# Kernel optimization log

Measured on AMD Instinct MI355X. Metric: run time of the kernel, lower is better.

Reference implementation:

```python
import jax, jax.numpy as jnp
import numpy as np

T, H, I, E, TOP_K = 1024, 1024, 512, 16, 4
SHARED_I = 512  # moe_intermediate_size * n_shared_experts


def setup_inputs() -> dict:
    key = jax.random.key(0)
    ks = jax.random.split(key, 6)
    s = 0.02
    return {
        "hidden_states": jax.random.normal(ks[0], (T, H), dtype=jnp.float32),
        "gate_w": jax.random.normal(ks[1], (E, H), dtype=jnp.float32) * s,          # router weight
        "w_gate_up": jax.random.normal(ks[2], (E, H, 2 * I), dtype=jnp.float32) * s,  # per-expert merged gate/up
        "w_down": jax.random.normal(ks[3], (E, I, H), dtype=jnp.float32) * s,
        "shared_gate_up": jax.random.normal(ks[4], (H, 2 * SHARED_I), dtype=jnp.float32) * s,
        "shared_down": jax.random.normal(ks[5], (SHARED_I, H), dtype=jnp.float32) * s,
    }


def _swiglu(gu):
    g, u = jnp.split(gu, 2, axis=-1)  # gate first, then up (SiluAndMul)
    return jax.nn.silu(g) * u


def reference(hidden_states, gate_w, w_gate_up, w_down, shared_gate_up, shared_down):
    x = hidden_states  # [T, H]
    # ---- router: sigmoid scoring, plain top-k (num_expert_group=topk_group=1), renormalize ----
    logits = x @ gate_w.T                      # [T, E]
    scores = jax.nn.sigmoid(logits)            # [T, E]
    topk_vals, topk_idx = jax.lax.top_k(scores, TOP_K)
    topk_w = topk_vals / jnp.sum(topk_vals, axis=-1, keepdims=True)
    # dense routing matrix [T, E] (zeros for unselected experts)
    route = jnp.zeros_like(scores).at[jnp.arange(T)[:, None], topk_idx].set(topk_w)
    # ---- routed experts: grouped SwiGLU GEMMs, combined by routing weights ----
    gu = jnp.einsum('th,ehf->etf', x, w_gate_up)   # [E, T, 2I]
    h = _swiglu(gu)                                 # [E, T, I]
    eo = jnp.einsum('eti,eih->eth', h, w_down)      # [E, T, H]
    routed = jnp.einsum('te,eth->th', route, eo)    # [T, H]
    # ---- shared expert (routed_scaling_factor = 1.0) ----
    shared = _swiglu(x @ shared_gate_up) @ shared_down  # [T, H]
    return routed + shared
```

## Files before the change

### kernel.cpp

```cpp
#include <hip/hip_runtime.h>
#include <hip/hip_bf16.h>
#include <cstdint>

#define T_TOK 1024
#define H_DIM 1024
#define I_DIM 512
#define E_NUM 16
#define TOPK  4

typedef __bf16 bf16;
typedef __bf16 bf16x4 __attribute__((ext_vector_type(4)));
typedef __bf16 bf16x8 __attribute__((ext_vector_type(8)));
typedef float  f32x4  __attribute__((ext_vector_type(4)));

#define GLOAD16(g, l)                                                                   \
  __builtin_amdgcn_global_load_lds((const __attribute__((address_space(1))) void*)(g),  \
                                   (__attribute__((address_space(3))) void*)(l), 16, 0, 0)

__device__ __forceinline__ unsigned lds_addr(const bf16* p) {
  return (unsigned)(uintptr_t)(const __attribute__((address_space(3))) bf16*)p;
}

template <int OFF>
__device__ __forceinline__ bf16x4 tr_read(unsigned addr) {
  bf16x4 r;
  if constexpr (OFF == 0)
    asm volatile("ds_read_b64_tr_b16 %0, %1" : "=v"(r) : "v"(addr));
  else if constexpr (OFF == 512)
    asm volatile("ds_read_b64_tr_b16 %0, %1 offset:512" : "=v"(r) : "v"(addr));
  else
    asm volatile("ds_read_b64_tr_b16 %0, %1 offset:1024" : "=v"(r) : "v"(addr));
  return r;
}

__device__ __forceinline__ bf16x8 cat8(bf16x4 a, bf16x4 b) {
  return __builtin_shufflevector(a, b, 0, 1, 2, 3, 4, 5, 6, 7);
}

__device__ __forceinline__ void conv_task(const float* __restrict__ src,
                                          bf16* __restrict__ dst, int lt, int tid) {
  const size_t b4 = (size_t)lt * 2048 + 2 * tid;
  const float4* s4 = (const float4*)src;
  float4 fa[4], fb[4];
#pragma unroll
  for (int p = 0; p < 4; ++p) {
    fa[p] = s4[b4 + (size_t)p * 512];
    fb[p] = s4[b4 + (size_t)p * 512 + 1];
  }
  bf16x8* d8 = (bf16x8*)dst;
#pragma unroll
  for (int p = 0; p < 4; ++p) {
    bf16x8 o;
    o[0]=(bf16)fa[p].x; o[1]=(bf16)fa[p].y; o[2]=(bf16)fa[p].z; o[3]=(bf16)fa[p].w;
    o[4]=(bf16)fb[p].x; o[5]=(bf16)fb[p].y; o[6]=(bf16)fb[p].z; o[7]=(bf16)fb[p].w;
    d8[(size_t)lt * 1024 + tid + (size_t)p * 256] = o;
  }
}

__global__ void prep_kernel(const float* __restrict__ x, bf16* __restrict__ xb,
                            const float* __restrict__ wgu, bf16* __restrict__ wguB,
                            const float* __restrict__ sgu, bf16* __restrict__ sguB,
                            const float* __restrict__ gw,
                            int* __restrict__ topk_e, float* __restrict__ topk_w,
                            int* __restrict__ counts, int* __restrict__ tok,
                            float* __restrict__ wt, int* __restrict__ slot) {
  const int b = blockIdx.x, tid = threadIdx.x;
  if (b < 1152) {
#pragma unroll
    for (int it = 0; it < 2; ++it) {
      const int task = b + it * 1152;
      if (task < 2048)      conv_task(wgu, wguB, task, tid);
      else if (task < 2176) conv_task(sgu, sguB, task - 2048, tid);
      else                  conv_task(x, xb, task - 2176, tid);
    }
  } else if (b < 1408) {
    const int wave = tid >> 6, lane = tid & 63;
    const int t = (b - 1152) * 4 + wave;
    const float4* xr = (const float4*)(x + (size_t)t * H_DIM);
    float4 xv[4];
#pragma unroll
    for (int j = 0; j < 4; ++j) xv[j] = xr[lane + 64 * j];
    float p[E_NUM];
#pragma unroll
    for (int e = 0; e < E_NUM; ++e) {
      const float4* gr = (const float4*)(gw + (size_t)e * H_DIM);
      float s = 0.f;
#pragma unroll
      for (int j = 0; j < 4; ++j) {
        float4 g = gr[lane + 64 * j];
        s += xv[j].x * g.x + xv[j].y * g.y + xv[j].z * g.z + xv[j].w * g.w;
      }
      p[e] = s;
    }
#pragma unroll
    for (int off = 32; off > 0; off >>= 1) {
#pragma unroll
      for (int e = 0; e < E_NUM; ++e) p[e] += __shfl_xor(p[e], off);
    }
    float rem[E_NUM];
#pragma unroll
    for (int e = 0; e < E_NUM; ++e) rem[e] = 1.f / (1.f + __expf(-p[e]));
    float vals[TOPK]; int idx[TOPK];
#pragma unroll
    for (int k = 0; k < TOPK; ++k) {
      float m = rem[0]; int mi = 0;
#pragma unroll
      for (int e = 1; e < E_NUM; ++e) {
        if (rem[e] > m) { m = rem[e]; mi = e; }
      }
      vals[k] = m; idx[k] = mi;
#pragma unroll
      for (int e = 0; e < E_NUM; ++e) rem[e] = (e == mi) ? -1e30f : rem[e];
    }
    if (lane == 0) {
      float inv = 1.f / (vals[0] + vals[1] + vals[2] + vals[3]);
      int4 ids; ids.x = idx[0]; ids.y = idx[1]; ids.z = idx[2]; ids.w = idx[3];
      float4 w4; w4.x = vals[0]*inv; w4.y = vals[1]*inv; w4.z = vals[2]*inv; w4.w = vals[3]*inv;
      ((int4*)topk_e)[t] = ids;
      ((float4*)topk_w)[t] = w4;
    }
  } else {
    const int i = (b - 1408) * 256 + tid;
    if (i == 0) counts[E_NUM] = T_TOK;
    tok [E_NUM * T_TOK + i] = i;
    wt  [E_NUM * T_TOK + i] = 1.0f;
    slot[E_NUM * T_TOK + i] = T_TOK * TOPK + i;
  }
}

__global__ void router_build_kernel(const int* __restrict__ topk_e, const float* __restrict__ topk_w,
                                    int* __restrict__ counts, int* __restrict__ tok,
                                    float* __restrict__ wt, int* __restrict__ slot) {
  const int e = blockIdx.x;
  const int tid = threadIdx.x, wave = tid >> 6, lane = tid & 63;
  __shared__ int wsum[4];
  int base = 0;
  for (int r = 0; r < 4; ++r) {
    int t = r * 256 + tid;
    int4 ids = ((const int4*)topk_e)[t];
    int match = -1;
    if (ids.x == e) match = 0;
    if (ids.y == e) match = 1;
    if (ids.z == e) match = 2;
    if (ids.w == e) match = 3;
    unsigned long long bm = __ballot(match >= 0);
    int prefix = __popcll(bm & ((1ull << lane) - 1ull));
    if (lane == 0) wsum[wave] = __popcll(bm);
    __syncthreads();
    int wbase = 0;
#pragma unroll
    for (int wv = 0; wv < 4; ++wv) wbase += (wv < wave) ? wsum[wv] : 0;
    int total = wsum[0] + wsum[1] + wsum[2] + wsum[3];
    if (match >= 0) {
      int pos = base + wbase + prefix;
      tok [e * T_TOK + pos] = t;
      wt  [e * T_TOK + pos] = topk_w[t * 4 + match];
      slot[e * T_TOK + pos] = t * 4 + match;
    }
    base += total;
    __syncthreads();
  }
  if (tid == 0) counts[e] = base;
}

__global__ __launch_bounds__(256, 4)
void gemm1_kernel(const bf16* __restrict__ xb, const bf16* __restrict__ wguB,
                  const bf16* __restrict__ sguB, const int* __restrict__ counts,
                  const int* __restrict__ tok, const float* __restrict__ wt,
                  const int* __restrict__ slot, bf16* __restrict__ hbuf,
                  const float* __restrict__ wdF, bf16* __restrict__ wdBo,
                  const float* __restrict__ sdF, bf16* __restrict__ sdBo) {
  const int tid = threadIdx.x;
  const int e = blockIdx.z;
  if (e >= 17) {
    const int cid = (e - 17) * 128 + blockIdx.y * 8 + blockIdx.x;
    if (cid < 1024)      conv_task(wdF, wdBo, cid, tid);
    else if (cid < 1088) conv_task(sdF, sdBo, cid - 1024, tid);
    return;
  }
  const int cnt = counts[e];
  const int rt  = blockIdx.y;
  if (rt * 64 >= cnt) return;
  const int nb = blockIdx.x * 64;
  const bf16* WB = (e < E_NUM) ? (wguB + (size_t)e * H_DIM * (2 * I_DIM)) : sguB;

  __shared__ __align__(16) bf16 sA[3][64 * 32];
  __shared__ __align__(16) bf16 sG[3][2048];
  __shared__ __align__(16) bf16 sU[3][2048];

  const int wave = tid >> 6, lane = tid & 63;
  const int wr = wave >> 1, wc = wave & 1;
  const int fr = lane & 15, kg = lane >> 4;
  const int lr = lane >> 2, lk = (lane & 3) * 8;

  int ar = rt * 64 + wave * 16 + lr;
  int arc = ar < cnt ? ar : cnt - 1;
  const bf16* aS = xb + (size_t)tok[e * T_TOK + arc] * H_DIM + lk;
  const int aOff = wave * 512;

  const int k_off = 8 * wave + 4 * (lane >> 5) + ((lane & 7) >> 1);
  const int n_off = 16 * ((lane >> 3) & 3) + 8 * (lane & 1);
  const bf16* gS = WB + (size_t)k_off * (2 * I_DIM) + nb + n_off;
  const bf16* uS = WB + (size_t)k_off * (2 * I_DIM) + I_DIM + nb + n_off;
  const int wOff = wave * 512;

  f32x4 accg[2][2], accu[2][2];
#pragma unroll
  for (int i = 0; i < 2; ++i)
#pragma unroll
    for (int j = 0; j < 2; ++j) { accg[i][j] = f32x4{0,0,0,0}; accu[i][j] = f32x4{0,0,0,0}; }

#define STG1(t, bidx) do { size_t ko = (size_t)(t) * 32;    \
    GLOAD16(aS + ko, sA[bidx] + aOff);                      \
    GLOAD16(gS + ko * (2 * I_DIM), sG[bidx] + wOff);        \
    GLOAD16(uS + ko * (2 * I_DIM), sU[bidx] + wOff); } while (0)

  STG1(0, 0); STG1(1, 1);
  const int NT = H_DIM / 32;
  int bufc = 0;
  for (int t = 0; t < NT; ++t) {
    int bn = bufc + 2; bn = bn >= 3 ? bn - 3 : bn;
    if (t + 2 < NT) {
      STG1(t + 2, bn);
      asm volatile("s_waitcnt vmcnt(6)" ::: "memory");
    } else if (t + 1 < NT) {
      asm volatile("s_waitcnt vmcnt(3)" ::: "memory");
    } else {
      asm volatile("s_waitcnt vmcnt(0)" ::: "memory");
    }
    __builtin_amdgcn_s_barrier();
    __builtin_amdgcn_sched_barrier(0);
    const bf16* A = sA[bufc];
    bf16x8 a0 = *(const bf16x8*)(A + (wr * 32      + fr) * 32 + kg * 8);
    bf16x8 a1 = *(const bf16x8*)(A + (wr * 32 + 16 + fr) * 32 + kg * 8);
    unsigned gb = lds_addr(sG[bufc]) + (unsigned)((lane >> 4) << 10) + (unsigned)((lane & 15) << 3);
    unsigned ub = lds_addr(sU[bufc]) + (unsigned)((lane >> 4) << 10) + (unsigned)((lane & 15) << 3);
    unsigned nb0 = (unsigned)(wc * 256), nb1 = nb0 + 128;
    bf16x8 g0 = cat8(tr_read<0>(gb + nb0), tr_read<512>(gb + nb0));
    bf16x8 g1 = cat8(tr_read<0>(gb + nb1), tr_read<512>(gb + nb1));
    bf16x8 u0 = cat8(tr_read<0>(ub + nb0), tr_read<512>(ub + nb0));
    bf16x8 u1 = cat8(tr_read<0>(ub + nb1), tr_read<512>(ub + nb1));
    asm volatile("s_waitcnt lgkmcnt(0)" ::: "memory");
    __builtin_amdgcn_sched_barrier(0);
    __builtin_amdgcn_s_setprio(1);
    accg[0][0] = __builtin_amdgcn_mfma_f32_16x16x32_bf16(a0, g0, accg[0][0], 0, 0, 0);
    accg[0][1] = __builtin_amdgcn_mfma_f32_16x16x32_bf16(a0, g1, accg[0][1], 0, 0, 0);
    accg[1][0] = __builtin_amdgcn_mfma_f32_16x16x32_bf16(a1, g0, accg[1][0], 0, 0, 0);
    accg[1][1] = __builtin_amdgcn_mfma_f32_16x16x32_bf16(a1, g1, accg[1][1], 0, 0, 0);
    accu[0][0] = __builtin_amdgcn_mfma_f32_16x16x32_bf16(a0, u0, accu[0][0], 0, 0, 0);
    accu[0][1] = __builtin_amdgcn_mfma_f32_16x16x32_bf16(a0, u1, accu[0][1], 0, 0, 0);
    accu[1][0] = __builtin_amdgcn_mfma_f32_16x16x32_bf16(a1, u0, accu[1][0], 0, 0, 0);
    accu[1][1] = __builtin_amdgcn_mfma_f32_16x16x32_bf16(a1, u1, accu[1][1], 0, 0, 0);
    __builtin_amdgcn_s_setprio(0);
    __builtin_amdgcn_sched_barrier(0);
    __builtin_amdgcn_s_barrier();
    bufc = bufc == 2 ? 0 : bufc + 1;
  }
#undef STG1

#pragma unroll
  for (int mi = 0; mi < 2; ++mi) {
#pragma unroll
    for (int j = 0; j < 4; ++j) {
      int grow = rt * 64 + wr * 32 + mi * 16 + kg * 4 + j;
      if (grow < cnt) {
        bf16* hr = hbuf + (size_t)slot[e * T_TOK + grow] * I_DIM;
        float w = wt[e * T_TOK + grow];
#pragma unroll
        for (int ni = 0; ni < 2; ++ni) {
          float g = accg[mi][ni][j], u = accu[mi][ni][j];
          float h = w * (g / (1.f + __expf(-g))) * u;
          hr[nb + wc * 32 + ni * 16 + fr] = (bf16)h;
        }
      }
    }
  }
}

__global__ __launch_bounds__(256, 4)
void gemm2_kernel(const bf16* __restrict__ hbuf, const bf16* __restrict__ wdB,
                  const bf16* __restrict__ sdB, const int* __restrict__ counts,
                  const int* __restrict__ slot, bf16* __restrict__ obuf) {
  const int e   = blockIdx.z;
  const int cnt = counts[e];
  const int rt  = blockIdx.y;
  if (rt * 64 >= cnt) return;
  const int nb = blockIdx.x * 128;
  const bf16* WB = (e < E_NUM) ? (wdB + (size_t)e * I_DIM * H_DIM) : sdB;

  __shared__ __align__(16) bf16 sA[3][64 * 32];
  __shared__ __align__(16) bf16 sB[3][4096];

  const int tid = threadIdx.x, wave = tid >> 6, lane = tid & 63;
  const int wr = wave >> 1, wc = wave & 1;
  const int fr = lane & 15, kg = lane >> 4;
  const int lr = lane >> 2, lk = (lane & 3) * 8;

  int ar = rt * 64 + wave * 16 + lr;
  int arc = ar < cnt ? ar : cnt - 1;
  const bf16* aS = hbuf + (size_t)slot[e * T_TOK + arc] * I_DIM + lk;
  const int aOff = wave * 512;

  const int j2 = (lane & 7) >> 1, h2 = lane & 1, nblk2 = lane >> 3;
  const int n2 = nb + nblk2 * 16 + 8 * h2;
  const bf16* bS0 = WB + (size_t)((wave * 2 + 0) * 4 + j2) * H_DIM + n2;
  const bf16* bS1 = WB + (size_t)((wave * 2 + 1) * 4 + j2) * H_DIM + n2;
  const int bOff0 = wave * 1024;
  const int bOff1 = bOff0 + 512;

  f32x4 acc[2][4];
#pragma unroll
  for (int i = 0; i < 2; ++i)
#pragma unroll
    for (int j = 0; j < 4; ++j) acc[i][j] = f32x4{0,0,0,0};

#define STG2(t, bidx) do { size_t ko = (size_t)(t) * 32;    \
    GLOAD16(aS + ko, sA[bidx] + aOff);                      \
    GLOAD16(bS0 + ko * H_DIM, sB[bidx] + bOff0);            \
    GLOAD16(bS1 + ko * H_DIM, sB[bidx] + bOff1); } while (0)

  STG2(0, 0); STG2(1, 1);
  const int NT = I_DIM / 32;
  int bufc = 0;
  for (int t = 0; t < NT; ++t) {
    int bn = bufc + 2; bn = bn >= 3 ? bn - 3 : bn;
    if (t + 2 < NT) {
      STG2(t + 2, bn);
      asm volatile("s_waitcnt vmcnt(6)" ::: "memory");
    } else if (t + 1 < NT) {
      asm volatile("s_waitcnt vmcnt(3)" ::: "memory");
    } else {
      asm volatile("s_waitcnt vmcnt(0)" ::: "memory");
    }
    __builtin_amdgcn_s_barrier();
    __builtin_amdgcn_sched_barrier(0);
    const bf16* A = sA[bufc];
    bf16x8 a0 = *(const bf16x8*)(A + (wr * 32      + fr) * 32 + kg * 8);
    bf16x8 a1 = *(const bf16x8*)(A + (wr * 32 + 16 + fr) * 32 + kg * 8);
    unsigned bb = lds_addr(sB[bufc]) + (unsigned)((lane >> 4) << 11) + (unsigned)((lane & 15) << 3)
                + (unsigned)(wc * 512);
    bf16x8 b[4];
#pragma unroll
    for (int ni = 0; ni < 4; ++ni)
      b[ni] = cat8(tr_read<0>(bb + ni * 128), tr_read<1024>(bb + ni * 128));
    asm volatile("s_waitcnt lgkmcnt(0)" ::: "memory");
    __builtin_amdgcn_sched_barrier(0);
    __builtin_amdgcn_s_setprio(1);
#pragma unroll
    for (int ni = 0; ni < 4; ++ni) {
      acc[0][ni] = __builtin_amdgcn_mfma_f32_16x16x32_bf16(a0, b[ni], acc[0][ni], 0, 0, 0);
      acc[1][ni] = __builtin_amdgcn_mfma_f32_16x16x32_bf16(a1, b[ni], acc[1][ni], 0, 0, 0);
    }
    __builtin_amdgcn_s_setprio(0);
    __builtin_amdgcn_sched_barrier(0);
    __builtin_amdgcn_s_barrier();
    bufc = bufc == 2 ? 0 : bufc + 1;
  }
#undef STG2

#pragma unroll
  for (int mi = 0; mi < 2; ++mi) {
#pragma unroll
    for (int j = 0; j < 4; ++j) {
      int grow = rt * 64 + wr * 32 + mi * 16 + kg * 4 + j;
      if (grow < cnt) {
        bf16* orow = obuf + (size_t)slot[e * T_TOK + grow] * H_DIM + nb + wc * 64 + fr;
#pragma unroll
        for (int ni = 0; ni < 4; ++ni)
          orow[ni * 16] = (bf16)acc[mi][ni][j];
      }
    }
  }
}

__global__ void reduce_kernel(const bf16* __restrict__ obuf, float* __restrict__ out) {
  const int t = blockIdx.x;
  const int c = threadIdx.x;
  const bf16x4* o4 = (const bf16x4*)obuf;
  float4 s; s.x = s.y = s.z = s.w = 0.f;
  int rows[5] = {t * 4, t * 4 + 1, t * 4 + 2, t * 4 + 3, T_TOK * TOPK + t};
#pragma unroll
  for (int r = 0; r < 5; ++r) {
    bf16x4 v = o4[(size_t)rows[r] * 256 + c];
    s.x += (float)v[0]; s.y += (float)v[1]; s.z += (float)v[2]; s.w += (float)v[3];
  }
  ((float4*)out)[(size_t)t * 256 + c] = s;
}

extern "C" void kernel_launch(void* const* d_in, const int* in_sizes, int n_in,
                              void* d_out, int out_size, void* d_ws, size_t ws_size,
                              hipStream_t stream) {
  const float* x   = (const float*)d_in[0];
  const float* gw  = (const float*)d_in[1];
  const float* wgu = (const float*)d_in[2];
  const float* wd  = (const float*)d_in[3];
  const float* sgu = (const float*)d_in[4];
  const float* sd  = (const float*)d_in[5];
  float* out = (float*)d_out;

  char* ws = (char*)d_ws;
  int*   counts = (int*)  (ws);
  int*   tok    = (int*)  (ws + 1024);
  float* wtA    = (float*)(ws + 70656);
  int*   slotA  = (int*)  (ws + 140288);
  int*   topk_e = (int*)  (ws + 209920);
  float* topk_w = (float*)(ws + 226304);
  bf16*  xb     = (bf16*) (ws + 245760);
  bf16*  hbuf   = (bf16*) (ws + 2342912);
  bf16*  wguB   = (bf16*) (ws + 7585792);
  bf16*  wdB    = (bf16*) (ws + 41140224);
  bf16*  sguB   = (bf16*) (ws + 57917440);
  bf16*  sdB    = (bf16*) (ws + 60014592);
  bf16*  obuf   = (bf16*) (ws + 7585792);

  prep_kernel<<<1412, 256, 0, stream>>>(x, xb, wgu, wguB, sgu, sguB,
                                        gw, topk_e, topk_w, counts, tok, wtA, slotA);
  router_build_kernel<<<E_NUM, 256, 0, stream>>>(topk_e, topk_w, counts, tok, wtA, slotA);
  gemm1_kernel<<<dim3(8, 16, 26), 256, 0, stream>>>(xb, wguB, sguB, counts, tok, wtA, slotA,
                                                    hbuf, wd, wdB, sd, sdB);
  gemm2_kernel<<<dim3(8, 16, 17), 256, 0, stream>>>(hbuf, wdB, sdB, counts, slotA, obuf);
  reduce_kernel<<<T_TOK, 256, 0, stream>>>(obuf, out);
}
```

Baseline: 85.48 us.

## Double K-step to 64 with two-stage buffering in gemm1 pipeline

Changes the gemm1 main loop from a triple-buffered 32-wide K step to a double-buffered 64-wide K step, issuing twice as many async global-to-LDS loads per stage and doing 16 MFMAs per barrier pair. This halves the number of barriers and waitcnt sync points per tile, at the cost of larger LDS footprint and more registers, so launch bounds drop to 3 blocks per CU. The refill is now issued after the trailing barrier rather than before the compute, so prefetch distance in time shrinks slightly.

```diff
diff --git a/kernel.cpp b/kernel.cpp
--- a/kernel.cpp
+++ b/kernel.cpp
@@ -163,7 +163,7 @@
   if (tid == 0) counts[e] = base;
 }
 
-__global__ __launch_bounds__(256, 4)
+__global__ __launch_bounds__(256, 3)
 void gemm1_kernel(const bf16* __restrict__ xb, const bf16* __restrict__ wguB,
                   const bf16* __restrict__ sguB, const int* __restrict__ counts,
                   const int* __restrict__ tok, const float* __restrict__ wt,
@@ -184,9 +184,9 @@
   const int nb = blockIdx.x * 64;
   const bf16* WB = (e < E_NUM) ? (wguB + (size_t)e * H_DIM * (2 * I_DIM)) : sguB;
 
-  __shared__ __align__(16) bf16 sA[3][64 * 32];
-  __shared__ __align__(16) bf16 sG[3][2048];
-  __shared__ __align__(16) bf16 sU[3][2048];
+  __shared__ __align__(16) bf16 sA[2][4096];
+  __shared__ __align__(16) bf16 sG[2][4096];
+  __shared__ __align__(16) bf16 sU[2][4096];
 
   const int wave = tid >> 6, lane = tid & 63;
   const int wr = wave >> 1, wc = wave & 1;
@@ -210,51 +210,62 @@
 #pragma unroll
     for (int j = 0; j < 2; ++j) { accg[i][j] = f32x4{0,0,0,0}; accu[i][j] = f32x4{0,0,0,0}; }
 
-#define STG1(t, bidx) do { size_t ko = (size_t)(t) * 32;    \
-    GLOAD16(aS + ko, sA[bidx] + aOff);                      \
-    GLOAD16(gS + ko * (2 * I_DIM), sG[bidx] + wOff);        \
-    GLOAD16(uS + ko * (2 * I_DIM), sU[bidx] + wOff); } while (0)
+#define STG1(t, bidx) do { size_t ko = (size_t)(t) * 64;            \
+    GLOAD16(aS + ko,      sA[bidx] + aOff);                         \
+    GLOAD16(aS + ko + 32, sA[bidx] + 2048 + aOff);                  \
+    GLOAD16(gS + ko * (2 * I_DIM),        sG[bidx] + wOff);         \
+    GLOAD16(gS + (ko + 32) * (2 * I_DIM), sG[bidx] + 2048 + wOff);  \
+    GLOAD16(uS + ko * (2 * I_DIM),        sU[bidx] + wOff);         \
+    GLOAD16(uS + (ko + 32) * (2 * I_DIM), sU[bidx] + 2048 + wOff); } while (0)
 
   STG1(0, 0); STG1(1, 1);
-  const int NT = H_DIM / 32;
-  int bufc = 0;
+  const int NT = H_DIM / 64;
   for (int t = 0; t < NT; ++t) {
-    int bn = bufc + 2; bn = bn >= 3 ? bn - 3 : bn;
-    if (t + 2 < NT) {
-      STG1(t + 2, bn);
-      asm volatile("s_waitcnt vmcnt(6)" ::: "memory");
-    } else if (t + 1 < NT) {
-      asm volatile("s_waitcnt vmcnt(3)" ::: "memory");
-    } else {
-      asm volatile("s_waitcnt vmcnt(0)" ::: "memory");
-    }
+    if (t + 1 < NT) asm volatile("s_waitcnt vmcnt(6)" ::: "memory");
+    else            asm volatile("s_waitcnt vmcnt(0)" ::: "memory");
     __builtin_amdgcn_s_barrier();
     __builtin_amdgcn_sched_barrier(0);
-    const bf16* A = sA[bufc];
-    bf16x8 a0 = *(const bf16x8*)(A + (wr * 32      + fr) * 32 + kg * 8);
-    bf16x8 a1 = *(const bf16x8*)(A + (wr * 32 + 16 + fr) * 32 + kg * 8);
-    unsigned gb = lds_addr(sG[bufc]) + (unsigned)((lane >> 4) << 10) + (unsigned)((lane & 15) << 3);
-    unsigned ub = lds_addr(sU[bufc]) + (unsigned)((lane >> 4) << 10) + (unsigned)((lane & 15) << 3);
+    const int buf = t & 1;
+    const bf16* A = sA[buf];
+    bf16x8 a0h0 = *(const bf16x8*)(A + (wr * 32      + fr) * 32 + kg * 8);
+    bf16x8 a1h0 = *(const bf16x8*)(A + (wr * 32 + 16 + fr) * 32 + kg * 8);
+    bf16x8 a0h1 = *(const bf16x8*)(A + 2048 + (wr * 32      + fr) * 32 + kg * 8);
+    bf16x8 a1h1 = *(const bf16x8*)(A + 2048 + (wr * 32 + 16 + fr) * 32 + kg * 8);
+    unsigned lb = (unsigned)((lane >> 4) << 10) + (unsigned)((lane & 15) << 3);
+    unsigned gb0 = lds_addr(sG[buf]) + lb, gb1 = gb0 + 4096;
+    unsigned ub0 = lds_addr(sU[buf]) + lb, ub1 = ub0 + 4096;
     unsigned nb0 = (unsigned)(wc * 256), nb1 = nb0 + 128;
-    bf16x8 g0 = cat8(tr_read<0>(gb + nb0), tr_read<512>(gb + nb0));
-    bf16x8 g1 = cat8(tr_read<0>(gb + nb1), tr_read<512>(gb + nb1));
-    bf16x8 u0 = cat8(tr_read<0>(ub + nb0), tr_read<512>(ub + nb0));
-    bf16x8 u1 = cat8(tr_read<0>(ub + nb1), tr_read<512>(ub + nb1));
+    bf16x8 g0h0 = cat8(tr_read<0>(gb0 + nb0), tr_read<512>(gb0 + nb0));
+    bf16x8 g1h0 = cat8(tr_read<0>(gb0 + nb1), tr_read<512>(gb0 + nb1));
+    bf16x8 u0h0 = cat8(tr_read<0>(ub0 + nb0), tr_read<512>(ub0 + nb0));
+    bf16x8 u1h0 = cat8(tr_read<0>(ub0 + nb1), tr_read<512>(ub0 + nb1));
+    bf16x8 g0h1 = cat8(tr_read<0>(gb1 + nb0), tr_read<512>(gb1 + nb0));
+    bf16x8 g1h1 = cat8(tr_read<0>(gb1 + nb1), tr_read<512>(gb1 + nb1));
+    bf16x8 u0h1 = cat8(tr_read<0>(ub1 + nb0), tr_read<512>(ub1 + nb0));
+    bf16x8 u1h1 = cat8(tr_read<0>(ub1 + nb1), tr_read<512>(ub1 + nb1));
     asm volatile("s_waitcnt lgkmcnt(0)" ::: "memory");
     __builtin_amdgcn_sched_barrier(0);
     __builtin_amdgcn_s_setprio(1);
-    accg[0][0] = __builtin_amdgcn_mfma_f32_16x16x32_bf16(a0, g0, accg[0][0], 0, 0, 0);
-    accg[0][1] = __builtin_amdgcn_mfma_f32_16x16x32_bf16(a0, g1, accg[0][1], 0, 0, 0);
-    accg[1][0] = __builtin_amdgcn_mfma_f32_16x16x32_bf16(a1, g0, accg[1][0], 0, 0, 0);
-    accg[1][1] = __builtin_amdgcn_mfma_f32_16x16x32_bf16(a1, g1, accg[1][1], 0, 0, 0);
-    accu[0][0] = __builtin_amdgcn_mfma_f32_16x16x32_bf16(a0, u0, accu[0][0], 0, 0, 0);
-    accu[0][1] = __builtin_amdgcn_mfma_f32_16x16x32_bf16(a0, u1, accu[0][1], 0, 0, 0);
-    accu[1][0] = __builtin_amdgcn_mfma_f32_16x16x32_bf16(a1, u0, accu[1][0], 0, 0, 0);
-    accu[1][1] = __builtin_amdgcn_mfma_f32_16x16x32_bf16(a1, u1, accu[1][1], 0, 0, 0);
+    accg[0][0] = __builtin_amdgcn_mfma_f32_16x16x32_bf16(a0h0, g0h0, accg[0][0], 0, 0, 0);
+    accg[0][1] = __builtin_amdgcn_mfma_f32_16x16x32_bf16(a0h0, g1h0, accg[0][1], 0, 0, 0);
+    accg[1][0] = __builtin_amdgcn_mfma_f32_16x16x32_bf16(a1h0, g0h0, accg[1][0], 0, 0, 0);
+    accg[1][1] = __builtin_amdgcn_mfma_f32_16x16x32_bf16(a1h0, g1h0, accg[1][1], 0, 0, 0);
+    accu[0][0] = __builtin_amdgcn_mfma_f32_16x16x32_bf16(a0h0, u0h0, accu[0][0], 0, 0, 0);
+    accu[0][1] = __builtin_amdgcn_mfma_f32_16x16x32_bf16(a0h0, u1h0, accu[0][1], 0, 0, 0);
+    accu[1][0] = __builtin_amdgcn_mfma_f32_16x16x32_bf16(a1h0, u0h0, accu[1][0], 0, 0, 0);
+    accu[1][1] = __builtin_amdgcn_mfma_f32_16x16x32_bf16(a1h0, u1h0, accu[1][1], 0, 0, 0);
+    accg[0][0] = __builtin_amdgcn_mfma_f32_16x16x32_bf16(a0h1, g0h1, accg[0][0], 0, 0, 0);
+    accg[0][1] = __builtin_amdgcn_mfma_f32_16x16x32_bf16(a0h1, g1h1, accg[0][1], 0, 0, 0);
+    accg[1][0] = __builtin_amdgcn_mfma_f32_16x16x32_bf16(a1h1, g0h1, accg[1][0], 0, 0, 0);
+    accg[1][1] = __builtin_amdgcn_mfma_f32_16x16x32_bf16(a1h1, g1h1, accg[1][1], 0, 0, 0);
+    accu[0][0] = __builtin_amdgcn_mfma_f32_16x16x32_bf16(a0h1, u0h1, accu[0][0], 0, 0, 0);
+    accu[0][1] = __builtin_amdgcn_mfma_f32_16x16x32_bf16(a0h1, u1h1, accu[0][1], 0, 0, 0);
+    accu[1][0] = __builtin_amdgcn_mfma_f32_16x16x32_bf16(a1h1, u0h1, accu[1][0], 0, 0, 0);
+    accu[1][1] = __builtin_amdgcn_mfma_f32_16x16x32_bf16(a1h1, u1h1, accu[1][1], 0, 0, 0);
     __builtin_amdgcn_s_setprio(0);
     __builtin_amdgcn_sched_barrier(0);
     __builtin_amdgcn_s_barrier();
-    bufc = bufc == 2 ? 0 : bufc + 1;
+    if (t + 2 < NT) STG1(t + 2, buf);
   }
 #undef STG1
 
```

Result: slower. 92.64 us (+8.4%).
